# Optimization experiments

Measured on AMD Instinct MI355X. Metric: run time of the kernel, lower is better.

Reference implementation:

```python
import jax, jax.numpy as jnp
import numpy as np

LN_EPS = 1e-5
NEG_INF = -1e30


def setup_inputs() -> dict:
    key = jax.random.key(0)
    k_adj, k_feat, k_mask, k_w = jax.random.split(key, 4)
    B, N, H, R, L = 8, 400, 768, 46, 2
    adj = jax.random.uniform(k_adj, (B, N, N, R), dtype=jnp.float32)
    feature = jax.random.normal(k_feat, (B, N, H), dtype=jnp.float32)
    dmask = (jax.random.uniform(k_mask, (B, 1, N)) > 0.1).astype(jnp.float32)
    # per-layer, per-relation Linear(H, H, bias=False) weights, applied as x @ W
    W = jax.random.normal(k_w, (L, R, H, H), dtype=jnp.float32) / np.sqrt(H)
    return {"adj": adj, "feature": feature, "dmask": dmask, "W": W}


def reference(adj, feature, dmask, W):
    # adj: [B,N,N,R] -> [B,R,N,N]; dmask: [B,1,N] masks key/column axis
    B, N, _, R = adj.shape
    a = jnp.transpose(adj, (0, 3, 1, 2))           # [B,R,N,N]
    m = dmask[:, None, :, :]                        # [B,1,1,N]
    logits = a * m + (1.0 - m) * NEG_INF
    att = jax.nn.softmax(logits, axis=-1)           # [B,R,N,N] (layer-invariant)

    x = feature
    num_layers = W.shape[0]
    for layer in range(num_layers):
        # grouped per-relation linear: h[b,r,n,k] = feature[b,n,h] @ W[layer,r,h,k]
        h = jnp.einsum('bnh,rhk->brnk', x, W[layer])
        h = jax.nn.relu(jnp.einsum('brnm,brmk->brnk', att, h))
        addition = h.sum(axis=1)                    # sum over relations -> [B,N,H]
        z = jax.nn.relu(addition) / R
        # LayerNorm without affine params
        mu = jnp.mean(z, axis=-1, keepdims=True)
        var = jnp.var(z, axis=-1, keepdims=True)
        x = (z - mu) / jnp.sqrt(var + LN_EPS)
        # dropout is identity in eval mode
    return x
```

## Files before the change

kernel.cpp:

```cpp
#include <hip/hip_runtime.h>
#include <stdint.h>

#define BS 8
#define NN 400
#define HH 768
#define RR 46
#define MB 416
#define APAD 448
#define MFLAT2 3328
#define LDW2 3328

typedef _Float16 half8 __attribute__((ext_vector_type(8)));
typedef _Float16 half4v __attribute__((ext_vector_type(4)));
typedef float floatx4 __attribute__((ext_vector_type(4)));

__device__ __forceinline__ void async16(const void* g, void* l) {
  __builtin_amdgcn_global_load_lds((const __attribute__((address_space(1))) uint32_t*)g,
                                   (__attribute__((address_space(3))) uint32_t*)l, 16, 0, 0);
}

__device__ __forceinline__ int xcd_work(int flat, int nwg) {
  int q = nwg >> 3, rem = nwg & 7;
  int xcd = flat & 7, slot = flat >> 3;
  return (xcd < rem ? xcd * (q + 1) : rem * (q + 1) + (xcd - rem) * q) + slot;
}

__device__ __forceinline__ void vm_wait(int ahead) {
  if (ahead >= 2) asm volatile("s_waitcnt vmcnt(8)" ::: "memory");
  else if (ahead == 1) asm volatile("s_waitcnt vmcnt(4)" ::: "memory");
  else asm volatile("s_waitcnt vmcnt(0)" ::: "memory");
}
__device__ __forceinline__ void vm_wait3(int ahead) {
  if (ahead >= 2) asm volatile("s_waitcnt vmcnt(6)" ::: "memory");
  else if (ahead == 1) asm volatile("s_waitcnt vmcnt(3)" ::: "memory");
  else asm volatile("s_waitcnt vmcnt(0)" ::: "memory");
}
#define BAR_ONE() { asm volatile("s_barrier" ::: "memory"); __builtin_amdgcn_sched_barrier(0); }


__device__ __forceinline__ void mma_tiles(const _Float16* As, const _Float16* Bs, int lane,
                                          int wr, int wc, floatx4 acc[4][4]) {
  int arow = wr + (lane & 15);
  int brow = wc + (lane & 15);
  int kswz = ((lane >> 4) ^ ((lane >> 1) & 3)) * 8;
  half8 a[4], b[4];
#pragma unroll
  for (int i = 0; i < 4; ++i) a[i] = *(const half8*)&As[(arow + i * 16) * 32 + kswz];
#pragma unroll
  for (int i = 0; i < 4; ++i) b[i] = *(const half8*)&Bs[(brow + i * 16) * 32 + kswz];
#pragma unroll
  for (int i = 0; i < 4; ++i)
#pragma unroll
    for (int j = 0; j < 4; ++j)
      acc[i][j] = __builtin_amdgcn_mfma_f32_16x16x32_f16(a[i], b[j], acc[i][j], 0, 0, 0);
}

__device__ __forceinline__ void mma32(const _Float16* As, const _Float16* Bs, int lane,
                                      int wr, int wc, floatx4 acc[8][4]) {
  int arow = wr + (lane & 15);
  int brow = wc + (lane & 15);
  int kswz = ((lane >> 4) ^ ((lane >> 1) & 3)) * 8;
  half8 a[8], b[4];
#pragma unroll
  for (int i = 0; i < 8; ++i) a[i] = *(const half8*)&As[(arow + i * 16) * 32 + kswz];
#pragma unroll
  for (int j = 0; j < 4; ++j) b[j] = *(const half8*)&Bs[(brow + j * 16) * 32 + kswz];
#pragma unroll
  for (int i = 0; i < 8; ++i)
#pragma unroll
    for (int j = 0; j < 4; ++j)
      acc[i][j] = __builtin_amdgcn_mfma_f32_16x16x32_f16(a[i], b[j], acc[i][j], 0, 0, 0);
}

__global__ __launch_bounds__(256) void conv_w(const float* __restrict__ W, _Float16* __restrict__ Wt) {
  __shared__ float tl[32][33];
  int t = threadIdx.x;
  int lr = blockIdx.y;
  int tr = blockIdx.x / 24, tc = blockIdx.x % 24;
  const float* src = W + (size_t)lr * HH * HH;
  _Float16* dst = Wt + (size_t)lr * HH * HH;
  int rl = t >> 5, cl = t & 31;
#pragma unroll
  for (int j = 0; j < 4; ++j)
    tl[rl + 8 * j][cl] = src[(size_t)(tr * 32 + rl + 8 * j) * HH + tc * 32 + cl];
  __syncthreads();
#pragma unroll
  for (int j = 0; j < 4; ++j)
    dst[(size_t)(tc * 32 + rl + 8 * j) * HH + tr * 32 + cl] = (_Float16)tl[cl][rl + 8 * j];
}

__global__ void conv_x(const float* __restrict__ f, _Float16* __restrict__ x16) {
  int i4 = blockIdx.x * 256 + threadIdx.x;
  int row = i4 / 192;
  int c4 = i4 - row * 192;
  int b = row / 416;
  int m = row - b * 416;
  half4v h = {};
  if (m < NN) {
    float4 v = *(const float4*)(f + ((size_t)(b * NN + m) * HH) + c4 * 4);
    h[0] = (_Float16)v.x; h[1] = (_Float16)v.y; h[2] = (_Float16)v.z; h[3] = (_Float16)v.w;
  }
  *(half4v*)&x16[(size_t)row * HH + c4 * 4] = h;
}

__global__ __launch_bounds__(512) void att_softmax(const float* __restrict__ adj,
                                                   const float* __restrict__ dmask,
                                                   _Float16* __restrict__ att) {
  __shared__ _Float16 sE[NN * RR];
  __shared__ float sM[NN];
  int t = threadIdx.x;
  int n = blockIdx.x, b = blockIdx.y;
  const float4* src = (const float4*)(adj + ((size_t)b * NN + n) * NN * RR);
  for (int i = t; i < NN; i += 512) sM[i] = dmask[b * NN + i];
  float4 v[9];
#pragma unroll
  for (int k = 0; k < 9; ++k) {
    int idx = t + k * 512;
    if (idx < NN * RR / 4) v[k] = src[idx];
  }
#pragma unroll
  for (int k = 0; k < 9; ++k) {
    int idx = t + k * 512;
    if (idx < NN * RR / 4) {
      half4v h;
      h[0] = (_Float16)__expf(v[k].x);
      h[1] = (_Float16)__expf(v[k].y);
      h[2] = (_Float16)__expf(v[k].z);
      h[3] = (_Float16)__expf(v[k].w);
      *(half4v*)&sE[idx * 4] = h;
    }
  }
  __syncthreads();
  int lane = t & 63, wid = t >> 6;
  for (int r = wid; r < RR; r += 8) {
    float s = 0.f;
    for (int m = lane; m < NN; m += 64)
      if (sM[m] > 0.5f) s += (float)sE[m * RR + r];
#pragma unroll
    for (int o = 32; o; o >>= 1) s += __shfl_xor(s, o);
    float inv = 1.0f / s;
    _Float16* orow = att + (((size_t)b * RR + r) * NN + n) * APAD;
    for (int m2 = lane * 2; m2 < APAD; m2 += 128) {
      _Float16 lo = (_Float16)0.f, hi = (_Float16)0.f;
      if (m2 < NN && sM[m2] > 0.5f) lo = (_Float16)((float)sE[m2 * RR + r] * inv);
      if (m2 + 1 < NN && sM[m2 + 1] > 0.5f) hi = (_Float16)((float)sE[(m2 + 1) * RR + r] * inv);
      union { _Float16 h[2]; uint32_t u; } pk;
      pk.h[0] = lo; pk.h[1] = hi;
      *(uint32_t*)&orow[m2] = pk.u;
    }
  }
}

__global__ __launch_bounds__(512, 2) void gemm_xw(const _Float16* __restrict__ x16,
                                                  const _Float16* __restrict__ Wt,
                                                  _Float16* __restrict__ h1T, int layer, int r0, int rbase) {
  extern __shared__ __align__(16) char smraw[];
  int t = threadIdx.x;
  int work = xcd_work(blockIdx.x, gridDim.x);
  int r_i = work / 39;
  int rem = work - r_i * 39;
  int r = r0 + r_i;
  int mtile = rem / 3, ntile = rem % 3;
  const _Float16* Bp = Wt + ((size_t)layer * RR + r) * HH * HH;
  int lane = t & 63, w = t >> 6;
  int wr = (w >> 2) * 128, wc = (w & 3) * 64;
  floatx4 acc[8][4] = {};

  int c0 = w * 2;
  int swz = ((lane & 3) ^ ((lane >> 3) & 3)) * 8;
  int ra0 = mtile * 256 + c0 * 16 + (lane >> 2);
  int ra1 = ra0 + 16;
  int rb0 = ntile * 256 + c0 * 16 + (lane >> 2);
  int rb1 = rb0 + 16;
  const _Float16* pa0 = x16 + (size_t)ra0 * HH + swz;
  const _Float16* pa1 = x16 + (size_t)ra1 * HH + swz;
  const _Float16* pb0 = Bp + (size_t)rb0 * HH + swz;
  const _Float16* pb1 = Bp + (size_t)rb1 * HH + swz;
  auto issue = [&](int buf) {
    _Float16* lA = (_Float16*)(smraw + (buf << 15)) + c0 * 512;
    _Float16* lB = (_Float16*)(smraw + (buf << 15) + 16384) + c0 * 512;
    async16(pa0, lA); async16(pa1, lA + 512);
    async16(pb0, lB); async16(pb1, lB + 512);
    pa0 += 32; pa1 += 32; pb0 += 32; pb1 += 32;
  };

  issue(0); issue(1); issue(2);
  vm_wait(2);
  BAR_ONE();
  for (int s = 0; s < 24; ++s) {
    if (s + 3 < 24) issue((s + 3) & 3);
    char* cb = smraw + ((s & 3) << 15);
    __builtin_amdgcn_s_setprio(1);
    mma32((const _Float16*)cb, (const _Float16*)(cb + 16384), lane, wr, wc, acc);
    __builtin_amdgcn_s_setprio(0);
    if (s + 1 < 24) {
      int ahead = 24 - s - 2;
      vm_wait(ahead > 2 ? 2 : ahead);
      BAR_ONE();
    }
  }
  __syncthreads();

  _Float16* outl = (_Float16*)smraw + (size_t)w * 8192;
#pragma unroll
  for (int i = 0; i < 8; ++i) {
#pragma unroll
    for (int j = 0; j < 4; ++j) {
      int rl = i * 16 + (lane >> 4) * 4;
      int cl = j * 16 + (lane & 15);
      int pos = rl ^ ((cl & 7) << 3);
      half4v v = {(_Float16)acc[i][j][0], (_Float16)acc[i][j][1],
                  (_Float16)acc[i][j][2], (_Float16)acc[i][j][3]};
      *(half4v*)&outl[cl * 128 + pos] = v;
    }
  }
  _Float16* outp = h1T + (size_t)(r - rbase) * HH * LDW2;
  int gmb = mtile * 256 + wr;
  int gnb = ntile * 256 + wc;
#pragma unroll
  for (int p = 0; p < 16; ++p) {
    int c = p * 4 + (lane >> 4);
    int mq = (lane & 15) * 8;
    int mpos = mq ^ ((c & 7) << 3);
    half8 v = *(const half8*)&outl[c * 128 + mpos];
    *(half8*)&outp[(size_t)(gnb + c) * LDW2 + gmb + mq] = v;
  }
}

__global__ __launch_bounds__(512, 2) void gemm_att(const _Float16* __restrict__ att,
                                                   const _Float16* __restrict__ h1T,
                                                   float* __restrict__ partials, size_t psz,
                                                   int rs, int rcount, int rbase, int accflag,
                                                   int ngroups) {
  extern __shared__ __align__(16) char smraw[];
  int t = threadIdx.x;
  int work = xcd_work(blockIdx.x, gridDim.x);
  int ntile = work % 6;
  int tmp = work / 6;
  int mtile = tmp & 1; tmp >>= 1;
  int g = tmp % ngroups;
  int b = tmp / ngroups;
  int rbeg = rs + (g * rcount) / ngroups;
  int rend = rs + ((g + 1) * rcount) / ngroups;
  int nr = rend - rbeg;
  int total = nr * 13;
  float* part = partials + (size_t)g * psz;
  int lane = t & 63, w = t >> 6;
  int wr = (w >> 1) * 64, wc = (w & 1) * 64;
  floatx4 acc[4][4] = {}, sum[4][4] = {};

  int swz = ((lane & 3) ^ ((lane >> 3) & 3)) * 8;
  int ga0 = mtile * 256 + w * 32 + (lane >> 2);
  int ga1 = ga0 + 16;
  ga0 = ga0 > NN - 1 ? NN - 1 : ga0;
  ga1 = ga1 > NN - 1 ? NN - 1 : ga1;
  int gb = ntile * 128 + w * 16 + (lane >> 2);
  const _Float16* pa0 = att + ((size_t)b * RR + rbeg) * NN * APAD + (size_t)ga0 * APAD + swz;
  const _Float16* pa1 = att + ((size_t)b * RR + rbeg) * NN * APAD + (size_t)ga1 * APAD + swz;
  const _Float16* pb = h1T + (size_t)(rbeg - rbase) * HH * LDW2 + (size_t)gb * LDW2 + b * MB + swz;
  int nsk = 0;
  auto issue = [&](int buf) {
    _Float16* lA = (_Float16*)(smraw + buf * 24576) + (w * 2) * 512;
    _Float16* lB = (_Float16*)(smraw + buf * 24576 + 16384) + w * 512;
    async16(pa0, lA); async16(pa1, lA + 512);
    async16(pb, lB);
    if (++nsk == 13) {
      nsk = 0;
      pa0 += (size_t)NN * APAD - 384; pa1 += (size_t)NN * APAD - 384;
      pb += (size_t)HH * LDW2 - 384;
    } else { pa0 += 32; pa1 += 32; pb += 32; }
  };

  issue(0); issue(1); issue(2);
  vm_wait3(2);
  BAR_ONE();
  int cks = 0;
  for (int s = 0; s < total; ++s) {
    if (s + 3 < total) issue((s + 3) & 3);
    char* cb = smraw + (s & 3) * 24576;
    __builtin_amdgcn_s_setprio(1);
    mma_tiles((const _Float16*)cb, (const _Float16*)(cb + 16384), lane, wr, wc, acc);
    __builtin_amdgcn_s_setprio(0);
    if (cks == 12) {
#pragma unroll
      for (int i = 0; i < 4; ++i)
#pragma unroll
        for (int j = 0; j < 4; ++j) {
#pragma unroll
          for (int q2 = 0; q2 < 4; ++q2) sum[i][j][q2] += fmaxf(acc[i][j][q2], 0.0f);
          acc[i][j] = (floatx4){0.f, 0.f, 0.f, 0.f};
        }
      cks = 0;
    } else ++cks;
    if (s + 1 < total) {
      int ahead = total - s - 2;
      vm_wait3(ahead > 2 ? 2 : ahead);
      BAR_ONE();
    }
  }
#pragma unroll
  for (int i = 0; i < 4; ++i) {
    int rl = wr + i * 16 + (lane >> 4) * 4;
    int grow = mtile * 256 + rl;
#pragma unroll
    for (int j = 0; j < 4; ++j) {
      int gcol = ntile * 128 + wc + j * 16 + (lane & 15);
#pragma unroll
      for (int q2 = 0; q2 < 4; ++q2) {
        if (grow + q2 < NN) {
          size_t idx = ((size_t)b * NN + grow + q2) * HH + gcol;
          float v = sum[i][j][q2];
          if (accflag) v += part[idx];
          part[idx] = v;
        }
      }
    }
  }
}

__global__ __launch_bounds__(256) void lnorm(const float* __restrict__ partials, size_t psz, int np,
                                             _Float16* __restrict__ x16, float* __restrict__ out) {
  int row = blockIdx.x;
  int t = threadIdx.x;
  int b = row / NN;
  int xrow = row + b * 16;
  float v[3];
  float s = 0.f, s2 = 0.f;
#pragma unroll
  for (int j = 0; j < 3; ++j) {
    float a = 0.f;
    for (int gidx = 0; gidx < np; ++gidx) a += partials[(size_t)gidx * psz + (size_t)row * HH + t + j * 256];
    v[j] = fmaxf(a, 0.f) * (1.0f / RR);
    s += v[j];
    s2 += v[j] * v[j];
  }
#pragma unroll
  for (int o = 32; o; o >>= 1) {
    s += __shfl_xor(s, o);
    s2 += __shfl_xor(s2, o);
  }
  __shared__ float rs_[4], rs2_[4];
  int lane = t & 63, wid = t >> 6;
  if (!lane) { rs_[wid] = s; rs2_[wid] = s2; }
  __syncthreads();
  s = rs_[0] + rs_[1] + rs_[2] + rs_[3];
  s2 = rs2_[0] + rs2_[1] + rs2_[2] + rs2_[3];
  float mu = s * (1.0f / HH);
  float var = s2 * (1.0f / HH) - mu * mu;
  float rstd = rsqrtf(var + 1e-5f);
#pragma unroll
  for (int j = 0; j < 3; ++j) {
    float o = (v[j] - mu) * rstd;
    out[(size_t)row * HH + t + j * 256] = o;
    x16[(size_t)xrow * HH + t + j * 256] = (_Float16)o;
  }
}

extern "C" void kernel_launch(void* const* d_in, const int* in_sizes, int n_in,
                              void* d_out, int out_size, void* d_ws, size_t ws_size,
                              hipStream_t stream) {
  const float* adj = (const float*)d_in[0];
  const float* feature = (const float*)d_in[1];
  const float* dmask = (const float*)d_in[2];
  const float* W = (const float*)d_in[3];
  float* out = (float*)d_out;

  (void)hipFuncSetAttribute((const void*)gemm_xw,
                            hipFuncAttributeMaxDynamicSharedMemorySize, 131072);
  (void)hipFuncSetAttribute((const void*)gemm_att,
                            hipFuncAttributeMaxDynamicSharedMemorySize, 98304);

  uintptr_t base = (uintptr_t)d_ws;
  uintptr_t p = base;
  auto alloc = [&](size_t bytes) -> void* {
    uintptr_t q = (p + 255) & ~(uintptr_t)255;
    p = q + bytes;
    return (void*)q;
  };
  _Float16* att = (_Float16*)alloc((size_t)BS * RR * NN * APAD * 2);
  _Float16* Wt = (_Float16*)alloc((size_t)2 * RR * HH * HH * 2);
  _Float16* x16 = (_Float16*)alloc((size_t)MFLAT2 * HH * 2);
  size_t psz = (size_t)(BS * NN) * HH;
  size_t pszB = psz * 4;
  size_t used = p - base;
  size_t rem = ws_size > used ? ws_size - used : 0;
  size_t perR = (size_t)HH * LDW2 * 2;
  size_t h1full = (size_t)RR * perR;

  conv_w<<<dim3(576, 2 * RR), 256, 0, stream>>>(W, Wt);
  conv_x<<<MFLAT2 * HH / 4 / 256, 256, 0, stream>>>(feature, x16);
  att_softmax<<<dim3(NN, BS), 512, 0, stream>>>(adj, dmask, att);

  if (rem >= h1full + 4 * pszB + 512) {
    _Float16* h1T = (_Float16*)alloc(h1full);
    int ngroups = (int)(((ws_size - (p - base)) - 256) / pszB);
    if (ngroups > 8) ngroups = 8;
    float* partials = (float*)alloc((size_t)ngroups * pszB);
    for (int layer = 0; layer < 2; ++layer) {
      gemm_xw<<<39 * RR, 512, 131072, stream>>>(x16, Wt, h1T, layer, 0, 0);
      gemm_att<<<96 * ngroups, 512, 98304, stream>>>(att, h1T, partials, psz, 0, RR, 0, 0, ngroups);
      lnorm<<<BS * NN, 256, 0, stream>>>(partials, psz, ngroups, x16, out);
    }
  } else {
    float* partials = (float*)alloc(pszB);
    size_t rem2 = ws_size > (p - base) ? ws_size - (p - base) : 0;
    int RCmax = (int)(rem2 / perR);
    if (RCmax > RR) RCmax = RR;
    if (RCmax < 1) RCmax = 1;
    _Float16* h1T = (_Float16*)alloc((size_t)RCmax * perR);
    for (int layer = 0; layer < 2; ++layer) {
      for (int r0 = 0; r0 < RR; r0 += RCmax) {
        int rc = RR - r0 < RCmax ? RR - r0 : RCmax;
        gemm_xw<<<39 * rc, 512, 131072, stream>>>(x16, Wt, h1T, layer, r0, r0);
        gemm_att<<<96 * 1, 512, 98304, stream>>>(att, h1T, partials, psz, r0, rc, r0, r0 > 0, 1);
      }
      lnorm<<<BS * NN, 256, 0, stream>>>(partials, psz, 1, x16, out);
    }
  }
}
```

Before: 980.5 us.

## Shrink gemm_xw N-tile to 128 with 3-stage pipeline for higher occupancy

Halves the gemm_xw output tile width from 256 to 128 columns, doubling the grid, and changes the LDS ring from 4 stages of 32KB to 3 stages of 24KB (72KB total). Launch bounds go to 4 blocks per CU, which lowers per-thread accumulator registers and is meant to let more waves overlap memory and MFMA work. In exchange, each A tile is reused across fewer columns, so global and LDS traffic per FLOP for x16 rises, and the prefetch distance shrinks from 3 to 2 stages.

```diff
diff --git a/kernel.cpp b/kernel.cpp
--- a/kernel.cpp
+++ b/kernel.cpp
@@ -25,11 +25,6 @@
   return (xcd < rem ? xcd * (q + 1) : rem * (q + 1) + (xcd - rem) * q) + slot;
 }
 
-__device__ __forceinline__ void vm_wait(int ahead) {
-  if (ahead >= 2) asm volatile("s_waitcnt vmcnt(8)" ::: "memory");
-  else if (ahead == 1) asm volatile("s_waitcnt vmcnt(4)" ::: "memory");
-  else asm volatile("s_waitcnt vmcnt(0)" ::: "memory");
-}
 __device__ __forceinline__ void vm_wait3(int ahead) {
   if (ahead >= 2) asm volatile("s_waitcnt vmcnt(6)" ::: "memory");
   else if (ahead == 1) asm volatile("s_waitcnt vmcnt(3)" ::: "memory");
@@ -55,20 +50,20 @@
       acc[i][j] = __builtin_amdgcn_mfma_f32_16x16x32_f16(a[i], b[j], acc[i][j], 0, 0, 0);
 }
 
-__device__ __forceinline__ void mma32(const _Float16* As, const _Float16* Bs, int lane,
-                                      int wr, int wc, floatx4 acc[8][4]) {
+__device__ __forceinline__ void mma16b(const _Float16* As, const _Float16* Bs, int lane,
+                                       int wr, int wc, floatx4 acc[8][2]) {
   int arow = wr + (lane & 15);
   int brow = wc + (lane & 15);
   int kswz = ((lane >> 4) ^ ((lane >> 1) & 3)) * 8;
-  half8 a[8], b[4];
+  half8 a[8], b[2];
 #pragma unroll
   for (int i = 0; i < 8; ++i) a[i] = *(const half8*)&As[(arow + i * 16) * 32 + kswz];
 #pragma unroll
-  for (int j = 0; j < 4; ++j) b[j] = *(const half8*)&Bs[(brow + j * 16) * 32 + kswz];
+  for (int j = 0; j < 2; ++j) b[j] = *(const half8*)&Bs[(brow + j * 16) * 32 + kswz];
 #pragma unroll
   for (int i = 0; i < 8; ++i)
 #pragma unroll
-    for (int j = 0; j < 4; ++j)
+    for (int j = 0; j < 2; ++j)
       acc[i][j] = __builtin_amdgcn_mfma_f32_16x16x32_f16(a[i], b[j], acc[i][j], 0, 0, 0);
 }
 
@@ -151,61 +146,60 @@
   }
 }
 
-__global__ __launch_bounds__(512, 2) void gemm_xw(const _Float16* __restrict__ x16,
+__global__ __launch_bounds__(512, 4) void gemm_xw(const _Float16* __restrict__ x16,
                                                   const _Float16* __restrict__ Wt,
                                                   _Float16* __restrict__ h1T, int layer, int r0, int rbase) {
   extern __shared__ __align__(16) char smraw[];
   int t = threadIdx.x;
   int work = xcd_work(blockIdx.x, gridDim.x);
-  int r_i = work / 39;
-  int rem = work - r_i * 39;
+  int r_i = work / 78;
+  int rem = work - r_i * 78;
   int r = r0 + r_i;
-  int mtile = rem / 3, ntile = rem % 3;
+  int mtile = rem / 6, ntile = rem % 6;
   const _Float16* Bp = Wt + ((size_t)layer * RR + r) * HH * HH;
   int lane = t & 63, w = t >> 6;
-  int wr = (w >> 2) * 128, wc = (w & 3) * 64;
-  floatx4 acc[8][4] = {};
-
-  int c0 = w * 2;
+  int wr = (w >> 2) * 128, wc = (w & 3) * 32;
+  floatx4 acc[8][2] = {};
+
   int swz = ((lane & 3) ^ ((lane >> 3) & 3)) * 8;
-  int ra0 = mtile * 256 + c0 * 16 + (lane >> 2);
-  int ra1 = ra0 + 16;
-  int rb0 = ntile * 256 + c0 * 16 + (lane >> 2);
-  int rb1 = rb0 + 16;
-  const _Float16* pa0 = x16 + (size_t)ra0 * HH + swz;
-  const _Float16* pa1 = x16 + (size_t)ra1 * HH + swz;
-  const _Float16* pb0 = Bp + (size_t)rb0 * HH + swz;
-  const _Float16* pb1 = Bp + (size_t)rb1 * HH + swz;
+  int ga0 = mtile * 256 + w * 32 + (lane >> 2);
+  int ga1 = ga0 + 16;
+  int gb = ntile * 128 + w * 16 + (lane >> 2);
+  const _Float16* pa0 = x16 + (size_t)ga0 * HH + swz;
+  const _Float16* pa1 = x16 + (size_t)ga1 * HH + swz;
+  const _Float16* pb = Bp + (size_t)gb * HH + swz;
   auto issue = [&](int buf) {
-    _Float16* lA = (_Float16*)(smraw + (buf << 15)) + c0 * 512;
-    _Float16* lB = (_Float16*)(smraw + (buf << 15) + 16384) + c0 * 512;
+    _Float16* lA = (_Float16*)(smraw + buf * 24576) + (w * 2) * 512;
+    _Float16* lB = (_Float16*)(smraw + buf * 24576 + 16384) + w * 512;
     async16(pa0, lA); async16(pa1, lA + 512);
-    async16(pb0, lB); async16(pb1, lB + 512);
-    pa0 += 32; pa1 += 32; pb0 += 32; pb1 += 32;
+    async16(pb, lB);
+    pa0 += 32; pa1 += 32; pb += 32;
   };
 
-  issue(0); issue(1); issue(2);
-  vm_wait(2);
+  issue(0); issue(1);
+  asm volatile("s_waitcnt vmcnt(3)" ::: "memory");
   BAR_ONE();
+  int cur = 0, nxt = 2;
   for (int s = 0; s < 24; ++s) {
-    if (s + 3 < 24) issue((s + 3) & 3);
-    char* cb = smraw + ((s & 3) << 15);
+    if (s + 2 < 24) { issue(nxt); nxt = nxt == 2 ? 0 : nxt + 1; }
+    char* cb = smraw + cur * 24576;
     __builtin_amdgcn_s_setprio(1);
-    mma32((const _Float16*)cb, (const _Float16*)(cb + 16384), lane, wr, wc, acc);
+    mma16b((const _Float16*)cb, (const _Float16*)(cb + 16384), lane, wr, wc, acc);
     __builtin_amdgcn_s_setprio(0);
     if (s + 1 < 24) {
-      int ahead = 24 - s - 2;
-      vm_wait(ahead > 2 ? 2 : ahead);
+      if (s + 2 < 24) { asm volatile("s_waitcnt vmcnt(3)" ::: "memory"); }
+      else            { asm volatile("s_waitcnt vmcnt(0)" ::: "memory"); }
       BAR_ONE();
     }
+    cur = cur == 2 ? 0 : cur + 1;
   }
   __syncthreads();
 
-  _Float16* outl = (_Float16*)smraw + (size_t)w * 8192;
+  _Float16* outl = (_Float16*)smraw + (size_t)w * 4096;
 #pragma unroll
   for (int i = 0; i < 8; ++i) {
 #pragma unroll
-    for (int j = 0; j < 4; ++j) {
+    for (int j = 0; j < 2; ++j) {
       int rl = i * 16 + (lane >> 4) * 4;
       int cl = j * 16 + (lane & 15);
       int pos = rl ^ ((cl & 7) << 3);
@@ -216,9 +210,9 @@
   }
   _Float16* outp = h1T + (size_t)(r - rbase) * HH * LDW2;
   int gmb = mtile * 256 + wr;
-  int gnb = ntile * 256 + wc;
-#pragma unroll
-  for (int p = 0; p < 16; ++p) {
+  int gnb = ntile * 128 + wc;
+#pragma unroll
+  for (int p = 0; p < 8; ++p) {
     int c = p * 4 + (lane >> 4);
     int mq = (lane & 15) * 8;
     int mpos = mq ^ ((c & 7) << 3);
@@ -366,7 +360,7 @@
   float* out = (float*)d_out;
 
   (void)hipFuncSetAttribute((const void*)gemm_xw,
-                            hipFuncAttributeMaxDynamicSharedMemorySize, 131072);
+                            hipFuncAttributeMaxDynamicSharedMemorySize, 73728);
   (void)hipFuncSetAttribute((const void*)gemm_att,
                             hipFuncAttributeMaxDynamicSharedMemorySize, 98304);
 
@@ -397,7 +391,7 @@
     if (ngroups > 8) ngroups = 8;
     float* partials = (float*)alloc((size_t)ngroups * pszB);
     for (int layer = 0; layer < 2; ++layer) {
-      gemm_xw<<<39 * RR, 512, 131072, stream>>>(x16, Wt, h1T, layer, 0, 0);
+      gemm_xw<<<78 * RR, 512, 73728, stream>>>(x16, Wt, h1T, layer, 0, 0);
       gemm_att<<<96 * ngroups, 512, 98304, stream>>>(att, h1T, partials, psz, 0, RR, 0, 0, ngroups);
       lnorm<<<BS * NN, 256, 0, stream>>>(partials, psz, ngroups, x16, out);
     }
@@ -411,7 +405,7 @@
     for (int layer = 0; layer < 2; ++layer) {
       for (int r0 = 0; r0 < RR; r0 += RCmax) {
         int rc = RR - r0 < RCmax ? RR - r0 : RCmax;
-        gemm_xw<<<39 * rc, 512, 131072, stream>>>(x16, Wt, h1T, layer, r0, r0);
+        gemm_xw<<<78 * rc, 512, 73728, stream>>>(x16, Wt, h1T, layer, r0, r0);
         gemm_att<<<96 * 1, 512, 98304, stream>>>(att, h1T, partials, psz, r0, rc, r0, r0 > 0, 1);
       }
       lnorm<<<BS * NN, 256, 0, stream>>>(partials, psz, 1, x16, out);
```

Result: faster. 961.0 us (-2.0%).
